# Kernel tuning notes

Measured on AMD Instinct MI355X. Metric: run time of the kernel, lower is better.

Reference implementation:

```python
import jax, jax.numpy as jnp
import numpy as np

# Dimensions (see shape_source)
IN_VEC = 131072          # input_vector_size
NUM_CAPS = 512           # num_capsules (output capsules)
CAP_SIZE = 256           # capsule_size
RF_SIZE = 64             # receptive_field_size
RF_PER_CAP = CAP_SIZE // RF_SIZE        # 4
IN_CAPS = IN_VEC // CAP_SIZE            # 512 input_eff_capsules
CONN_P = 0.1             # connection_probability


def setup_inputs() -> dict:
    key = jax.random.key(0)
    kx, kc, kw = jax.random.split(key, 3)
    x = jax.random.normal(kx, (IN_VEC,), dtype=jnp.float32)
    # Sparse ScRRAMBLe routing tensor: mostly zeros, gated by connection probability.
    # Shape (input_eff_capsules, rf_per_cap_in, num_capsules, rf_per_cap_out) per einsum 'ijkl,ijm->klm'.
    Ci = (jax.random.uniform(kc, (IN_CAPS, RF_PER_CAP, NUM_CAPS, RF_PER_CAP)) < CONN_P).astype(jnp.float32)
    # glorot_normal over last two axes: fan_in = fan_out = RF_SIZE -> std = sqrt(2/(64+64)) = 0.125
    glorot_std = float(np.sqrt(2.0 / (RF_SIZE + RF_SIZE)))
    Wi = glorot_std * jax.random.normal(kw, (NUM_CAPS, RF_PER_CAP, RF_PER_CAP, RF_SIZE, RF_SIZE), dtype=jnp.float32)
    return {"x": x, "Ci": Ci, "Wi": Wi}


def reference(x, Ci, Wi):
    # x: (IN_VEC,) -> (input_eff_capsules, rf_per_cap, rf_size)
    x_reshaped = x.reshape(IN_CAPS, RF_PER_CAP, RF_SIZE)
    # Route input receptive fields to output capsule slots:
    # x_routed: (num_capsules, rf_per_cap, rf_size)
    x_routed = jnp.einsum('ijkl,ijm->klm', Ci, x_reshaped)
    # Per-capsule small batched transform:
    # y: (num_capsules, rf_per_cap, rf_size)
    y = jnp.einsum('ijklm,ikm->ijl', Wi, x_routed)
    return y
```

## Files before the change

kernel.cpp:

```cpp
#include <hip/hip_runtime.h>


typedef float f4 __attribute__((ext_vector_type(4)));

#define NCH 8

__global__ __launch_bounds__(256) void route_kernel(
    const float* __restrict__ x,
    const float* __restrict__ Ci,
    float* __restrict__ xr_part)
{
    const int iq  = blockIdx.x;
    const int c   = blockIdx.y;
    const int t   = threadIdx.x;
    const int il  = t >> 6;
    const int g   = (t >> 4) & 3;
    const int mq4 = t & 15;
    const int i   = (iq << 2) + il;

    const f4* __restrict__ Ci4 = (const f4*)Ci;
    const f4* __restrict__ x4  = (const f4*)x;

    __shared__ f4 part[1024];

    f4 a0 = {0.f,0.f,0.f,0.f};
    f4 a1 = {0.f,0.f,0.f,0.f};
    f4 a2 = {0.f,0.f,0.f,0.f};
    f4 a3 = {0.f,0.f,0.f,0.f};

    const int ijpc = 2048 / NCH;
    const int sub  = ijpc >> 2;
    const int base = c * ijpc + g * sub;
    #pragma unroll 4
    for (int it = 0; it < sub; ++it) {
        const int ij = base + it;
        const f4 c4 = Ci4[ij * 512 + i];
        const f4 xv = x4[(ij << 4) + mq4];
        a0 += c4.x * xv;
        a1 += c4.y * xv;
        a2 += c4.z * xv;
        a3 += c4.w * xv;
    }

    const int pb = ((g << 2) + il) << 2;
    part[(pb + 0) * 16 + mq4] = a0;
    part[(pb + 1) * 16 + mq4] = a1;
    part[(pb + 2) * 16 + mq4] = a2;
    part[(pb + 3) * 16 + mq4] = a3;
    __syncthreads();

    const int il2 = t >> 6;
    const int r   = (t >> 4) & 3;
    const int mm  = t & 15;
    f4 s = {0.f,0.f,0.f,0.f};
    #pragma unroll
    for (int gg = 0; gg < 4; ++gg)
        s += part[(((gg << 2) + il2) * 4 + r) * 16 + mm];

    f4* __restrict__ xp4 = (f4*)xr_part;
    xp4[(c * 512 + (iq << 2) + il2) * 64 + r * 16 + mm] = s;
}

__global__ __launch_bounds__(256, 4) void transform_kernel(
    const float* __restrict__ Wi,
    const float* __restrict__ xr_part,
    float* __restrict__ y)
{
    const int b    = blockIdx.x;
    const int i    = b >> 2;
    const int t    = threadIdx.x;
    const int lane = t & 63;
    const int w    = t >> 6;
    const int lq   = lane >> 4;
    const int m16  = lane & 15;

    const f4* __restrict__ W4 = (const f4*)Wi;
    const int wbase = b * 4096;
    const int lw    = w << 4;

    f4 wv[16];
    #pragma unroll
    for (int c2 = 0; c2 < 4; ++c2) {
        const int l = lw + (c2 << 2) + lq;
        #pragma unroll
        for (int k = 0; k < 4; ++k)
            wv[(c2 << 2) + k] =
                __builtin_nontemporal_load(&W4[wbase + (k << 10) + l * 16 + m16]);
    }

    const f4* __restrict__ xp4 = (const f4*)xr_part;
    f4 xr0 = {0.f,0.f,0.f,0.f};
    f4 xr1 = {0.f,0.f,0.f,0.f};
    f4 xr2 = {0.f,0.f,0.f,0.f};
    f4 xr3 = {0.f,0.f,0.f,0.f};
    #pragma unroll
    for (int c = 0; c < NCH; ++c) {
        const int base = (c * 512 + i) * 64;
        xr0 += xp4[base + 0 * 16 + m16];
        xr1 += xp4[base + 1 * 16 + m16];
        xr2 += xp4[base + 2 * 16 + m16];
        xr3 += xp4[base + 3 * 16 + m16];
    }

    #pragma unroll
    for (int c2 = 0; c2 < 4; ++c2) {
        const int l = lw + (c2 << 2) + lq;
        f4 s = wv[(c2 << 2) + 0] * xr0
             + wv[(c2 << 2) + 1] * xr1
             + wv[(c2 << 2) + 2] * xr2
             + wv[(c2 << 2) + 3] * xr3;
        float p = s.x + s.y + s.z + s.w;
        p += __shfl_xor(p, 1);
        p += __shfl_xor(p, 2);
        p += __shfl_xor(p, 4);
        p += __shfl_xor(p, 8);
        if (m16 == 0) y[b * 64 + l] = p;
    }
}

extern "C" void kernel_launch(void* const* d_in, const int* in_sizes, int n_in,
                              void* d_out, int out_size, void* d_ws, size_t ws_size,
                              hipStream_t stream) {
    const float* x  = (const float*)d_in[0];
    const float* Ci = (const float*)d_in[1];
    const float* Wi = (const float*)d_in[2];
    float* y  = (float*)d_out;
    float* xr = (float*)d_ws;

    route_kernel<<<dim3(128, NCH), 256, 0, stream>>>(x, Ci, xr);
    transform_kernel<<<2048, 256, 0, stream>>>(Wi, xr, y);
}
```

Measured before the change: 223.4 us.

## Stream Wi through double-buffered LDS with direct global-to-LDS loads

Instead of each thread pulling its 16 Wi vectors into registers with nontemporal loads, the transform kernel streams each 16KB k-slice of Wi into a double-buffered shared-memory tile using global_load_lds. While one slice is being fetched, the previous one is multiplied against the routed input, aiming to overlap memory and compute and to cut register pressure. The cost is block barriers, 32KB of LDS per block that limits occupancy, and dropping the nontemporal cache hint and the occupancy hint in launch_bounds.

Result: no change. 227.6 us (+1.9%).

```diff
diff --git a/kernel.cpp b/kernel.cpp
--- a/kernel.cpp
+++ b/kernel.cpp
@@ -61,11 +61,20 @@
     xp4[(c * 512 + (iq << 2) + il2) * 64 + r * 16 + mm] = s;
 }
 
-__global__ __launch_bounds__(256, 4) void transform_kernel(
+__device__ __forceinline__ void gload_lds16(const float* g, float* l) {
+    __builtin_amdgcn_global_load_lds(
+        (const __attribute__((address_space(1))) unsigned int*)g,
+        (__attribute__((address_space(3))) unsigned int*)l,
+        16, 0, 0);
+}
+
+__global__ __launch_bounds__(256) void transform_kernel(
     const float* __restrict__ Wi,
     const float* __restrict__ xr_part,
     float* __restrict__ y)
 {
+    __shared__ float lds[2][4096];
+
     const int b    = blockIdx.x;
     const int i    = b >> 2;
     const int t    = threadIdx.x;
@@ -74,19 +83,11 @@
     const int lq   = lane >> 4;
     const int m16  = lane & 15;
 
-    const f4* __restrict__ W4 = (const f4*)Wi;
-    const int wbase = b * 4096;
-    const int lw    = w << 4;
+    const float* Wb = Wi + (size_t)b * 16384;
 
-    f4 wv[16];
     #pragma unroll
-    for (int c2 = 0; c2 < 4; ++c2) {
-        const int l = lw + (c2 << 2) + lq;
-        #pragma unroll
-        for (int k = 0; k < 4; ++k)
-            wv[(c2 << 2) + k] =
-                __builtin_nontemporal_load(&W4[wbase + (k << 10) + l * 16 + m16]);
-    }
+    for (int p = 0; p < 4; ++p)
+        gload_lds16(Wb + 0 * 4096 + p * 1024 + t * 4, &lds[0][p * 1024 + t * 4]);
 
     const f4* __restrict__ xp4 = (const f4*)xr_part;
     f4 xr0 = {0.f,0.f,0.f,0.f};
@@ -102,19 +103,66 @@
         xr3 += xp4[base + 3 * 16 + m16];
     }
 
+    f4 acc0 = {0.f,0.f,0.f,0.f};
+    f4 acc1 = {0.f,0.f,0.f,0.f};
+    f4 acc2 = {0.f,0.f,0.f,0.f};
+    f4 acc3 = {0.f,0.f,0.f,0.f};
+
+    const f4* buf0 = (const f4*)lds[0];
+    const f4* buf1 = (const f4*)lds[1];
+    const int ro = (w << 8) + lane;
+
+    __syncthreads();
+
     #pragma unroll
-    for (int c2 = 0; c2 < 4; ++c2) {
-        const int l = lw + (c2 << 2) + lq;
-        f4 s = wv[(c2 << 2) + 0] * xr0
-             + wv[(c2 << 2) + 1] * xr1
-             + wv[(c2 << 2) + 2] * xr2
-             + wv[(c2 << 2) + 3] * xr3;
-        float p = s.x + s.y + s.z + s.w;
-        p += __shfl_xor(p, 1);
-        p += __shfl_xor(p, 2);
-        p += __shfl_xor(p, 4);
-        p += __shfl_xor(p, 8);
-        if (m16 == 0) y[b * 64 + l] = p;
+    for (int p = 0; p < 4; ++p)
+        gload_lds16(Wb + 1 * 4096 + p * 1024 + t * 4, &lds[1][p * 1024 + t * 4]);
+    acc0 += buf0[ro +   0] * xr0;
+    acc1 += buf0[ro +  64] * xr0;
+    acc2 += buf0[ro + 128] * xr0;
+    acc3 += buf0[ro + 192] * xr0;
+    __syncthreads();
+
+    #pragma unroll
+    for (int p = 0; p < 4; ++p)
+        gload_lds16(Wb + 2 * 4096 + p * 1024 + t * 4, &lds[0][p * 1024 + t * 4]);
+    acc0 += buf1[ro +   0] * xr1;
+    acc1 += buf1[ro +  64] * xr1;
+    acc2 += buf1[ro + 128] * xr1;
+    acc3 += buf1[ro + 192] * xr1;
+    __syncthreads();
+
+    #pragma unroll
+    for (int p = 0; p < 4; ++p)
+        gload_lds16(Wb + 3 * 4096 + p * 1024 + t * 4, &lds[1][p * 1024 + t * 4]);
+    acc0 += buf0[ro +   0] * xr2;
+    acc1 += buf0[ro +  64] * xr2;
+    acc2 += buf0[ro + 128] * xr2;
+    acc3 += buf0[ro + 192] * xr2;
+    __syncthreads();
+
+    acc0 += buf1[ro +   0] * xr3;
+    acc1 += buf1[ro +  64] * xr3;
+    acc2 += buf1[ro + 128] * xr3;
+    acc3 += buf1[ro + 192] * xr3;
+
+    float p0 = acc0.x + acc0.y + acc0.z + acc0.w;
+    float p1 = acc1.x + acc1.y + acc1.z + acc1.w;
+    float p2 = acc2.x + acc2.y + acc2.z + acc2.w;
+    float p3 = acc3.x + acc3.y + acc3.z + acc3.w;
+    #pragma unroll
+    for (int d = 1; d < 16; d <<= 1) {
+        p0 += __shfl_xor(p0, d);
+        p1 += __shfl_xor(p1, d);
+        p2 += __shfl_xor(p2, d);
+        p3 += __shfl_xor(p3, d);
+    }
+    if (m16 == 0) {
+        const int lbase = b * 64 + (w << 4) + lq;
+        y[lbase +  0] = p0;
+        y[lbase +  4] = p1;
+        y[lbase +  8] = p2;
+        y[lbase + 12] = p3;
     }
 }
 
```

## Stream Wi with flat coalesced loads and atomic accumulation of outputs

Applied to the files above, without the earlier changes.

The per-block transform, which loaded a 64 KB Wi tile into registers, becomes a grid-stride stream over Wi. Each 16-lane group does a dot product against the routed input and atomically adds it into y. A separate kernel first reduces the route partial sums into a compact xr buffer, and y is zeroed with a memset. The aim is more memory-level parallelism and better DRAM streaming on the dominant Wi read. The cost is an extra launch, a memset, and four float atomics per output element, which makes the summation order nondeterministic.

Measured after the change: 225.3 us. No clear change (+0.8%).

```diff
diff --git a/kernel.cpp b/kernel.cpp
--- a/kernel.cpp
+++ b/kernel.cpp
@@ -61,60 +61,47 @@
     xp4[(c * 512 + (iq << 2) + il2) * 64 + r * 16 + mm] = s;
 }
 
-__global__ __launch_bounds__(256, 4) void transform_kernel(
+__global__ __launch_bounds__(256) void reduce_xr_kernel(
+    const float* __restrict__ xr_part,
+    float* __restrict__ xr)
+{
+    const int t = blockIdx.x * 256 + threadIdx.x;
+    const f4* __restrict__ p4 = (const f4*)xr_part;
+    f4 s = {0.f,0.f,0.f,0.f};
+    #pragma unroll
+    for (int c = 0; c < NCH; ++c) s += p4[c * 32768 + t];
+    ((f4*)xr)[t] = s;
+}
+
+__global__ __launch_bounds__(256) void transform_stream(
     const float* __restrict__ Wi,
-    const float* __restrict__ xr_part,
+    const float* __restrict__ xr,
     float* __restrict__ y)
 {
-    const int b    = blockIdx.x;
-    const int i    = b >> 2;
-    const int t    = threadIdx.x;
-    const int lane = t & 63;
-    const int w    = t >> 6;
-    const int lq   = lane >> 4;
-    const int m16  = lane & 15;
+    const int tid  = blockIdx.x * 256 + threadIdx.x;
+    const int m16  = threadIdx.x & 15;
 
-    const f4* __restrict__ W4 = (const f4*)Wi;
-    const int wbase = b * 4096;
-    const int lw    = w << 4;
+    const f4* __restrict__ W4  = (const f4*)Wi;
+    const f4* __restrict__ xr4 = (const f4*)xr;
 
-    f4 wv[16];
-    #pragma unroll
-    for (int c2 = 0; c2 < 4; ++c2) {
-        const int l = lw + (c2 << 2) + lq;
-        #pragma unroll
-        for (int k = 0; k < 4; ++k)
-            wv[(c2 << 2) + k] =
-                __builtin_nontemporal_load(&W4[wbase + (k << 10) + l * 16 + m16]);
-    }
-
-    const f4* __restrict__ xp4 = (const f4*)xr_part;
-    f4 xr0 = {0.f,0.f,0.f,0.f};
-    f4 xr1 = {0.f,0.f,0.f,0.f};
-    f4 xr2 = {0.f,0.f,0.f,0.f};
-    f4 xr3 = {0.f,0.f,0.f,0.f};
-    #pragma unroll
-    for (int c = 0; c < NCH; ++c) {
-        const int base = (c * 512 + i) * 64;
-        xr0 += xp4[base + 0 * 16 + m16];
-        xr1 += xp4[base + 1 * 16 + m16];
-        xr2 += xp4[base + 2 * 16 + m16];
-        xr3 += xp4[base + 3 * 16 + m16];
-    }
-
-    #pragma unroll
-    for (int c2 = 0; c2 < 4; ++c2) {
-        const int l = lw + (c2 << 2) + lq;
-        f4 s = wv[(c2 << 2) + 0] * xr0
-             + wv[(c2 << 2) + 1] * xr1
-             + wv[(c2 << 2) + 2] * xr2
-             + wv[(c2 << 2) + 3] * xr3;
-        float p = s.x + s.y + s.z + s.w;
+    #pragma unroll 4
+    for (int it = 0; it < 32; ++it) {
+        const int idx = it * 262144 + tid;
+        const f4 w = W4[idx];
+        const int row = idx >> 4;
+        const int i   = row >> 10;
+        const int k   = (row >> 6) & 3;
+        const f4 xv = xr4[i * 64 + k * 16 + m16];
+        const f4 s4 = w * xv;
+        float p = s4.x + s4.y + s4.z + s4.w;
         p += __shfl_xor(p, 1);
         p += __shfl_xor(p, 2);
         p += __shfl_xor(p, 4);
         p += __shfl_xor(p, 8);
-        if (m16 == 0) y[b * 64 + l] = p;
+        if (m16 == 0) {
+            const int yi = ((row >> 8) << 6) | (row & 63);
+            atomicAdd(&y[yi], p);
+        }
     }
 }
 
@@ -124,9 +111,12 @@
     const float* x  = (const float*)d_in[0];
     const float* Ci = (const float*)d_in[1];
     const float* Wi = (const float*)d_in[2];
-    float* y  = (float*)d_out;
-    float* xr = (float*)d_ws;
+    float* y       = (float*)d_out;
+    float* xr_part = (float*)d_ws;
+    float* xr      = (float*)d_ws + NCH * 512 * 256;
 
-    route_kernel<<<dim3(128, NCH), 256, 0, stream>>>(x, Ci, xr);
-    transform_kernel<<<2048, 256, 0, stream>>>(Wi, xr, y);
+    hipMemsetAsync(y, 0, (size_t)out_size * sizeof(float), stream);
+    route_kernel<<<dim3(128, NCH), 256, 0, stream>>>(x, Ci, xr_part);
+    reduce_xr_kernel<<<128, 256, 0, stream>>>(xr_part, xr);
+    transform_stream<<<1024, 256, 0, stream>>>(Wi, xr, y);
 }
```
